# Optimization experiments

Measured on AMD Instinct MI355X. Metric: run time of the kernel, lower is better.

Reference implementation:

```python
import jax, jax.numpy as jnp
import numpy as np

N, E = 50000, 1600000
IN_DIM, HID, HEADS, DH, NCLS = 1280, 256, 4, 64, 6
NEG_SLOPE = 0.2
LN_EPS = 1e-5


def setup_inputs() -> dict:
    key = jax.random.key(0)
    ks = jax.random.split(key, 24)
    p = {}
    p['x'] = jax.random.normal(ks[0], (N, IN_DIM), dtype=jnp.float32)
    p['edge_index'] = jax.random.randint(ks[1], (2, E), 0, N, dtype=jnp.int64)
    s = 0.05
    p['W_in'] = jax.random.normal(ks[2], (IN_DIM, HID), dtype=jnp.float32) * s
    p['b_in'] = jnp.zeros((HID,), jnp.float32)
    for l in range(2):
        p[f'W_gat{l}'] = jax.random.normal(ks[3 + 6 * l], (HID, HEADS * DH), dtype=jnp.float32) * s
        p[f'att_src{l}'] = jax.random.normal(ks[4 + 6 * l], (HEADS, DH), dtype=jnp.float32) * s
        p[f'att_dst{l}'] = jax.random.normal(ks[5 + 6 * l], (HEADS, DH), dtype=jnp.float32) * s
        p[f'b_gat{l}'] = jnp.zeros((HEADS * DH,), jnp.float32)
        p[f'ln_g{l}'] = jnp.ones((HID,), jnp.float32)
        p[f'ln_b{l}'] = jnp.zeros((HID,), jnp.float32)
    p['W_c1'] = jax.random.normal(ks[20], (HID, HID // 2), dtype=jnp.float32) * s
    p['b_c1'] = jnp.zeros((HID // 2,), jnp.float32)
    p['W_c2'] = jax.random.normal(ks[21], (HID // 2, NCLS), dtype=jnp.float32) * s
    p['b_c2'] = jnp.zeros((NCLS,), jnp.float32)
    return p


def _layer_norm(h, g, b):
    mu = jnp.mean(h, axis=-1, keepdims=True)
    var = jnp.mean((h - mu) ** 2, axis=-1, keepdims=True)
    return (h - mu) * jax.lax.rsqrt(var + LN_EPS) * g + b


def _gat_conv(h, src, dst, W, a_src, a_dst, bias):
    # h: [N, HID] -> per-head projections [N, H, DH]
    xh = (h @ W).reshape(N, HEADS, DH)
    al_src = jnp.sum(xh * a_src, axis=-1)  # [N, H]
    al_dst = jnp.sum(xh * a_dst, axis=-1)  # [N, H]
    e = jax.nn.leaky_relu(al_src[src] + al_dst[dst], NEG_SLOPE)  # [E', H]
    # edge softmax over incoming edges of each destination node
    m = jax.ops.segment_max(e, dst, num_segments=N)
    e = jnp.exp(e - m[dst])
    denom = jax.ops.segment_sum(e, dst, num_segments=N)
    w = e / denom[dst]  # [E', H]
    msg = xh[src] * w[:, :, None]  # [E', H, DH]
    out = jax.ops.segment_sum(msg, dst, num_segments=N)  # [N, H, DH]
    return out.reshape(N, HEADS * DH) + bias


def reference(x, edge_index, W_in, b_in, W_gat0, att_src0, att_dst0, b_gat0, ln_g0, ln_b0,
              W_gat1, att_src1, att_dst1, b_gat1, ln_g1, ln_b1, W_c1, b_c1, W_c2, b_c2):
    # add self loops (PyG GATConv default)
    loop = jnp.arange(N, dtype=edge_index.dtype)
    src = jnp.concatenate([edge_index[0], loop])
    dst = jnp.concatenate([edge_index[1], loop])

    h = jax.nn.relu(x @ W_in + b_in)

    for (Wg, asrc, adst, bg, g, b) in ((W_gat0, att_src0, att_dst0, b_gat0, ln_g0, ln_b0),
                                       (W_gat1, att_src1, att_dst1, b_gat1, ln_g1, ln_b1)):
        h_new = _gat_conv(h, src, dst, Wg, asrc, adst, bg)
        h_new = jax.nn.relu(_layer_norm(h_new, g, b))
        h = h + h_new

    logits = jax.nn.relu(h @ W_c1 + b_c1) @ W_c2 + b_c2
    return logits
```

## Files before the change

### kernel.cpp

```cpp
#include <hip/hip_runtime.h>

#define NN 50000
#define EE 1600000
#define INDIM 1280
#define HID 256
#define HEADS 4
#define DHD 64
#define NCLS 6
#define NEG 0.2f
#define LNEPS 1e-5f

typedef __attribute__((ext_vector_type(8))) short short8;
typedef __attribute__((ext_vector_type(4))) float floatx4;

__device__ __forceinline__ unsigned short f2b(float f) {
    unsigned int u = __float_as_uint(f);
    u += 0x7FFF + ((u >> 16) & 1);
    return (unsigned short)(u >> 16);
}
__device__ __forceinline__ float b2f(unsigned short b) {
    return __uint_as_float(((unsigned int)b) << 16);
}

#define WAIT_LGKM0() __builtin_amdgcn_s_waitcnt(0xC07F)

__global__ void init_cnt_kernel(int* __restrict__ cnt) {
    int n = blockIdx.x * 256 + threadIdx.x;
    if (n < NN) cnt[n] = 1;
}

__global__ void count_edges_kernel(const int* __restrict__ dst, int* __restrict__ cnt) {
    int e = blockIdx.x * 256 + threadIdx.x;
    if (e < EE) atomicAdd(&cnt[dst[e]], 1);
}

__global__ __launch_bounds__(1024) void scan1_kernel(const int* __restrict__ cnt,
                                                     int* __restrict__ scanned,
                                                     int* __restrict__ chtot, int n) {
    __shared__ int wsum[16];
    int tid = threadIdx.x, lane = tid & 63, wv = tid >> 6;
    int i = blockIdx.x * 1024 + tid;
    int s = (i < n) ? cnt[i] : 0;
#pragma unroll
    for (int off = 1; off < 64; off <<= 1) {
        int t = __shfl_up(s, off, 64);
        if (lane >= off) s += t;
    }
    if (lane == 63) wsum[wv] = s;
    __syncthreads();
    if (tid < 16) {
        int ws = wsum[tid];
#pragma unroll
        for (int off = 1; off < 16; off <<= 1) {
            int t = __shfl_up(ws, off, 16);
            if (tid >= off) ws += t;
        }
        wsum[tid] = ws;
    }
    __syncthreads();
    s += (wv > 0) ? wsum[wv - 1] : 0;
    if (i < n) scanned[i] = s;
    if (tid == 1023) chtot[blockIdx.x] = s;
}

__global__ void scan2_kernel(int* __restrict__ chtot, int nch) {
    int lane = threadIdx.x;
    int v = (lane < nch) ? chtot[lane] : 0;
#pragma unroll
    for (int off = 1; off < 64; off <<= 1) {
        int t = __shfl_up(v, off, 64);
        if (lane >= off) v += t;
    }
    if (lane < nch) chtot[lane] = v;
}

__global__ void scan3_kernel(const int* __restrict__ scanned, const int* __restrict__ chtot,
                             int* __restrict__ rowptr, int n) {
    int i = blockIdx.x * 256 + threadIdx.x;
    if (i == 0) rowptr[0] = 0;
    if (i < n) {
        int ch = i >> 10;
        rowptr[i + 1] = scanned[i] + (ch ? chtot[ch - 1] : 0);
    }
}

__global__ void copyfill_kernel(const int* __restrict__ rowptr, int* __restrict__ cursor,
                                int* __restrict__ csr) {
    int n = blockIdx.x * 256 + threadIdx.x;
    if (n < NN) {
        int p = rowptr[n];
        csr[p] = n;
        cursor[n] = p + 1;
    }
}

__global__ void scatter_edges_kernel(const int* __restrict__ src, const int* __restrict__ dst,
                                     int* __restrict__ cursor, int* __restrict__ csr) {
    int e = blockIdx.x * 256 + threadIdx.x;
    if (e < EE) {
        int d = dst[e];
        int pos = atomicAdd(&cursor[d], 1);
        csr[pos] = src[e];
    }
}

__global__ void pack_w_kernel(const float* __restrict__ W, unsigned short* __restrict__ out,
                              int K, int N) {
    int idx = blockIdx.x * 256 + threadIdx.x;
    int total = (K >> 6) * (N >> 4) * 2 * 64;
    if (idx >= total) return;
    int ln = idx & 63;
    int t = idx >> 6;
    int ks = t & 1; t >>= 1;
    int NT = N >> 4;
    int nt = t % NT, kc = t / NT;
    int n = nt * 16 + (ln & 15);
    int k = kc * 64 + ks * 32 + ((ln >> 4) << 3);
    unsigned short u[8];
#pragma unroll
    for (int j = 0; j < 8; j++) u[j] = f2b(W[(size_t)(k + j) * N + n]);
    *(int4*)&out[(size_t)idx * 8] = *(const int4*)u;
}

template <int AF32, int KI, int NT, int ACT, int WF32, int WB16, int PROJ, int CLS>
__global__ __launch_bounds__(256) void pgemm_kernel(const float* __restrict__ Af,
                                                    const unsigned short* __restrict__ Ab,
                                                    const unsigned short* __restrict__ Bf,
                                                    const float* __restrict__ bias,
                                                    float* __restrict__ Cf,
                                                    unsigned short* __restrict__ Cb,
                                                    const float* __restrict__ aps,
                                                    const float* __restrict__ apd,
                                                    float* __restrict__ als,
                                                    float* __restrict__ ald,
                                                    const float* __restrict__ W2,
                                                    const float* __restrict__ b2,
                                                    float* __restrict__ out2,
                                                    int M) {
    constexpr int NW = NT / 4;
    constexpr int K = KI * 64;
    __shared__ __align__(16) unsigned short Als[2][4096];
    int tid = threadIdx.x, wv = tid >> 6, ln = tid & 63;
    int m0 = blockIdx.x * 64;

    int srow[2], scol[2];
#pragma unroll
    for (int i = 0; i < 2; i++) {
        int s = tid + i * 256;
        int r = s >> 3;
        srow[i] = min(m0 + r, M - 1);
        scol[i] = ((s & 7) ^ (r & 7)) * 8;
    }

    floatx4 acc[4][NW] = {};
    short8 breg[2][NW * 2];
    float4 af0[4], af1[4];
    int4 ai0[2], ai1[2];

    auto issueA = [&](int k, float4* af, int4* ai) {
#pragma unroll
        for (int i = 0; i < 2; i++) {
            if (AF32) {
                const float* p = Af + (size_t)srow[i] * K + k * 64 + scol[i];
                af[i * 2] = *(const float4*)p;
                af[i * 2 + 1] = *(const float4*)(p + 4);
            } else {
                ai[i] = *(const int4*)(Ab + (size_t)srow[i] * K + k * 64 + scol[i]);
            }
        }
    };
    auto issueB = [&](int k, short8* b) {
#pragma unroll
        for (int nw = 0; nw < NW; nw++)
#pragma unroll
            for (int ks = 0; ks < 2; ks++)
                b[nw * 2 + ks] = *(const short8*)(
                    Bf + ((((size_t)k * NT + (wv * NW + nw)) * 2 + ks) * 64 + ln) * 8);
    };
    auto writeA = [&](int k, const float4* af, const int4* ai) {
        unsigned short* dst = &Als[k & 1][0];
#pragma unroll
        for (int i = 0; i < 2; i++) {
            int4 v;
            if (AF32) {
                unsigned short u[8] = {f2b(af[2 * i].x), f2b(af[2 * i].y),
                                       f2b(af[2 * i].z), f2b(af[2 * i].w),
                                       f2b(af[2 * i + 1].x), f2b(af[2 * i + 1].y),
                                       f2b(af[2 * i + 1].z), f2b(af[2 * i + 1].w)};
                v = *(const int4*)u;
            } else {
                v = ai[i];
            }
            *(int4*)&dst[(tid + i * 256) * 8] = v;
        }
    };
    auto compute = [&](int k, const short8* b) {
        const unsigned short* src = &Als[k & 1][0];
#pragma unroll
        for (int ks = 0; ks < 2; ks++) {
            short8 a[4];
#pragma unroll
            for (int mt = 0; mt < 4; mt++) {
                int row = mt * 16 + (ln & 15);
                int g = ks * 4 + (ln >> 4);
                int off8 = (row >> 3) * 512 + (row & 7) * 64 + (g ^ (row & 7)) * 8;
                a[mt] = *(const short8*)&src[off8];
            }
#pragma unroll
            for (int nw = 0; nw < NW; nw++)
#pragma unroll
                for (int mt = 0; mt < 4; mt++)
                    acc[mt][nw] = __builtin_amdgcn_mfma_f32_16x16x32_bf16(
                        a[mt], b[nw * 2 + ks], acc[mt][nw], 0, 0, 0);
        }
    };

    issueA(0, af0, ai0);
    issueB(0, breg[0]);
    writeA(0, af0, ai0);
    WAIT_LGKM0();
    __builtin_amdgcn_s_barrier();

#pragma unroll
    for (int kk = 0; kk < KI / 2; kk++) {
        int k = kk * 2;
        issueA(k + 1, af1, ai1);
        issueB(k + 1, breg[1]);
        compute(k, breg[0]);
        writeA(k + 1, af1, ai1);
        WAIT_LGKM0();
        __builtin_amdgcn_s_barrier();
        if (k + 2 < KI) {
            issueA(k + 2, af0, ai0);
            issueB(k + 2, breg[0]);
        }
        compute(k + 1, breg[1]);
        if (k + 2 < KI) {
            writeA(k + 2, af0, ai0);
            WAIT_LGKM0();
            __builtin_amdgcn_s_barrier();
        }
    }

    constexpr int Nout = NT * 16;
    if constexpr (WF32 || WB16) {
#pragma unroll
        for (int mt = 0; mt < 4; mt++) {
#pragma unroll
            for (int nw = 0; nw < NW; nw++) {
                int col = (wv * NW + nw) * 16 + (ln & 15);
                int rb = m0 + mt * 16 + (ln >> 4) * 4;
                float bi = bias ? bias[col] : 0.f;
#pragma unroll
                for (int r = 0; r < 4; r++) {
                    int row = rb + r;
                    if (row < M) {
                        float v = acc[mt][nw][r] + bi;
                        if (ACT) v = fmaxf(v, 0.f);
                        if (WF32) Cf[(size_t)row * Nout + col] = v;
                        if (WB16) Cb[(size_t)row * Nout + col] = f2b(v);
                    }
                }
            }
        }
    }

    if constexpr (PROJ) {
        float avs[NW], avd[NW];
#pragma unroll
        for (int nw = 0; nw < NW; nw++) {
            int d = nw * 16 + (ln & 15);
            avs[nw] = aps[wv * DHD + d];
            avd[nw] = apd[wv * DHD + d];
        }
#pragma unroll
        for (int mt = 0; mt < 4; mt++) {
#pragma unroll
            for (int r = 0; r < 4; r++) {
                float ssum = 0.f, dsum = 0.f;
#pragma unroll
                for (int nw = 0; nw < NW; nw++) {
                    float v = acc[mt][nw][r];
                    ssum = fmaf(v, avs[nw], ssum);
                    dsum = fmaf(v, avd[nw], dsum);
                }
#pragma unroll
                for (int m = 8; m > 0; m >>= 1) {
                    ssum += __shfl_xor(ssum, m, 16);
                    dsum += __shfl_xor(dsum, m, 16);
                }
                int row = m0 + mt * 16 + (ln >> 4) * 4 + r;
                if ((ln & 15) == 0 && row < M) {
                    als[row * 4 + wv] = ssum;
                    ald[row * 4 + wv] = dsum;
                }
            }
        }
    }

    if constexpr (CLS) {
        __shared__ float cred[64][4][NCLS];
        float w2[NW][NCLS];
#pragma unroll
        for (int nw = 0; nw < NW; nw++) {
            int col = (wv * NW + nw) * 16 + (ln & 15);
#pragma unroll
            for (int c = 0; c < NCLS; c++) w2[nw][c] = W2[col * NCLS + c];
        }
#pragma unroll
        for (int mt = 0; mt < 4; mt++) {
#pragma unroll
            for (int r = 0; r < 4; r++) {
                float p[NCLS] = {};
#pragma unroll
                for (int nw = 0; nw < NW; nw++) {
                    int col = (wv * NW + nw) * 16 + (ln & 15);
                    float v = fmaxf(acc[mt][nw][r] + bias[col], 0.f);
#pragma unroll
                    for (int c = 0; c < NCLS; c++) p[c] = fmaf(v, w2[nw][c], p[c]);
                }
#pragma unroll
                for (int m = 8; m > 0; m >>= 1)
#pragma unroll
                    for (int c = 0; c < NCLS; c++) p[c] += __shfl_xor(p[c], m, 16);
                int rl = mt * 16 + (ln >> 4) * 4 + r;
                if ((ln & 15) == 0)
#pragma unroll
                    for (int c = 0; c < NCLS; c++) cred[rl][wv][c] = p[c];
            }
        }
        __syncthreads();
        for (int t = tid; t < 64 * NCLS; t += 256) {
            int row = t / NCLS, c = t % NCLS;
            if (m0 + row < M) {
                float s = cred[row][0][c] + cred[row][1][c] + cred[row][2][c] +
                          cred[row][3][c] + b2[c];
                out2[(size_t)(m0 + row) * NCLS + c] = s;
            }
        }
    }
}

__global__ __launch_bounds__(256) void agg_ln_kernel(const int* __restrict__ rowptr,
                                                     const int* __restrict__ csr,
                                                     const float* __restrict__ al_s,
                                                     const float* __restrict__ al_d,
                                                     const unsigned short* __restrict__ xhb,
                                                     const float* __restrict__ bgat,
                                                     const float* __restrict__ g,
                                                     const float* __restrict__ bb,
                                                     float* __restrict__ h,
                                                     unsigned short* __restrict__ hb) {
    int wv = threadIdx.x >> 6, ln = threadIdx.x & 63;
    int n = blockIdx.x * 4 + wv;
    if (n >= NN) return;
    int start = rowptr[n], end = rowptr[n + 1];
    float4 ad = *(const float4*)&al_d[n * 4];

    float d0 = 0.f, d1 = 0.f, d2 = 0.f, d3 = 0.f;
    for (int i = start + ln; i < end; i += 64) {
        int s = csr[i];
        float4 as = *(const float4*)&al_s[s * 4];
        float e0 = as.x + ad.x; e0 = e0 > 0.f ? e0 : NEG * e0;
        float e1 = as.y + ad.y; e1 = e1 > 0.f ? e1 : NEG * e1;
        float e2 = as.z + ad.z; e2 = e2 > 0.f ? e2 : NEG * e2;
        float e3 = as.w + ad.w; e3 = e3 > 0.f ? e3 : NEG * e3;
        d0 += __expf(e0); d1 += __expf(e1); d2 += __expf(e2); d3 += __expf(e3);
    }
#pragma unroll
    for (int off = 32; off > 0; off >>= 1) {
        d0 += __shfl_xor(d0, off, 64);
        d1 += __shfl_xor(d1, off, 64);
        d2 += __shfl_xor(d2, off, 64);
        d3 += __shfl_xor(d3, off, 64);
    }
    int myh = ln >> 4;
    float invh = 1.f / ((myh == 0) ? d0 : (myh == 1) ? d1 : (myh == 2) ? d2 : d3);
    float adh = (myh == 0) ? ad.x : (myh == 1) ? ad.y : (myh == 2) ? ad.z : ad.w;

    float p0 = 0.f, p1 = 0.f, p2 = 0.f, p3 = 0.f;
    float q0 = 0.f, q1 = 0.f, q2 = 0.f, q3 = 0.f;
    int i = start;
    for (; i + 1 < end; i += 2) {
        int s0 = csr[i], s1 = csr[i + 1];
        float e0 = al_s[s0 * 4 + myh] + adh; e0 = e0 > 0.f ? e0 : NEG * e0;
        float e1 = al_s[s1 * 4 + myh] + adh; e1 = e1 > 0.f ? e1 : NEG * e1;
        float w0 = __expf(e0) * invh;
        float w1 = __expf(e1) * invh;
        ushort4 u0 = *(const ushort4*)&xhb[(size_t)s0 * HID + ln * 4];
        ushort4 u1 = *(const ushort4*)&xhb[(size_t)s1 * HID + ln * 4];
        p0 = fmaf(w0, b2f(u0.x), p0); q0 = fmaf(w1, b2f(u1.x), q0);
        p1 = fmaf(w0, b2f(u0.y), p1); q1 = fmaf(w1, b2f(u1.y), q1);
        p2 = fmaf(w0, b2f(u0.z), p2); q2 = fmaf(w1, b2f(u1.z), q2);
        p3 = fmaf(w0, b2f(u0.w), p3); q3 = fmaf(w1, b2f(u1.w), q3);
    }
    if (i < end) {
        int s0 = csr[i];
        float e0 = al_s[s0 * 4 + myh] + adh; e0 = e0 > 0.f ? e0 : NEG * e0;
        float w0 = __expf(e0) * invh;
        ushort4 u0 = *(const ushort4*)&xhb[(size_t)s0 * HID + ln * 4];
        p0 = fmaf(w0, b2f(u0.x), p0);
        p1 = fmaf(w0, b2f(u0.y), p1);
        p2 = fmaf(w0, b2f(u0.z), p2);
        p3 = fmaf(w0, b2f(u0.w), p3);
    }
    float a0 = p0 + q0, a1 = p1 + q1, a2 = p2 + q2, a3 = p3 + q3;

    float4 bg = *(const float4*)&bgat[ln * 4];
    float v0 = a0 + bg.x, v1 = a1 + bg.y, v2 = a2 + bg.z, v3 = a3 + bg.w;
    float ps = v0 + v1 + v2 + v3;
    float ps2 = v0 * v0 + v1 * v1 + v2 * v2 + v3 * v3;
#pragma unroll
    for (int off = 32; off > 0; off >>= 1) {
        ps += __shfl_xor(ps, off, 64);
        ps2 += __shfl_xor(ps2, off, 64);
    }
    float mu = ps * (1.f / HID);
    float var = ps2 * (1.f / HID) - mu * mu;
    float rs = rsqrtf(var + LNEPS);
    float4 gg = *(const float4*)&g[ln * 4];
    float4 bbv = *(const float4*)&bb[ln * 4];
    float o0 = fmaxf((v0 - mu) * rs * gg.x + bbv.x, 0.f);
    float o1 = fmaxf((v1 - mu) * rs * gg.y + bbv.y, 0.f);
    float o2 = fmaxf((v2 - mu) * rs * gg.z + bbv.z, 0.f);
    float o3 = fmaxf((v3 - mu) * rs * gg.w + bbv.w, 0.f);
    size_t idx = (size_t)n * HID + ln * 4;
    float4 hv = *(const float4*)&h[idx];
    float4 nh = make_float4(hv.x + o0, hv.y + o1, hv.z + o2, hv.w + o3);
    *(float4*)&h[idx] = nh;
    ushort4 nb = {f2b(nh.x), f2b(nh.y), f2b(nh.z), f2b(nh.w)};
    *(ushort4*)&hb[idx] = nb;
}

extern "C" void kernel_launch(void* const* d_in, const int* in_sizes, int n_in,
                              void* d_out, int out_size, void* d_ws, size_t ws_size,
                              hipStream_t stream) {
    const float* x    = (const float*)d_in[0];
    const int*   ei   = (const int*)d_in[1];
    const float* W_in = (const float*)d_in[2];
    const float* b_in = (const float*)d_in[3];
    const float* W_gat[2]   = {(const float*)d_in[4],  (const float*)d_in[10]};
    const float* att_src[2] = {(const float*)d_in[5],  (const float*)d_in[11]};
    const float* att_dst[2] = {(const float*)d_in[6],  (const float*)d_in[12]};
    const float* b_gat[2]   = {(const float*)d_in[7],  (const float*)d_in[13]};
    const float* ln_g[2]    = {(const float*)d_in[8],  (const float*)d_in[14]};
    const float* ln_b[2]    = {(const float*)d_in[9],  (const float*)d_in[15]};
    const float* W_c1 = (const float*)d_in[16];
    const float* b_c1 = (const float*)d_in[17];
    const float* W_c2 = (const float*)d_in[18];
    const float* b_c2 = (const float*)d_in[19];

    char* ws = (char*)d_ws;
    size_t off = 0;
    auto alloc = [&](size_t bytes) -> void* {
        void* p = ws + off;
        off += (bytes + 255) & ~(size_t)255;
        return p;
    };
    float*          h   = (float*)alloc((size_t)NN * HID * 4);
    unsigned short* hb  = (unsigned short*)alloc((size_t)NN * HID * 2);
    unsigned short* xhb = (unsigned short*)alloc((size_t)NN * HID * 2);
    float* al_s = (float*)alloc((size_t)NN * HEADS * 4);
    float* al_d = (float*)alloc((size_t)NN * HEADS * 4);
    int* rowptr  = (int*)alloc((size_t)(NN + 1) * 4);
    int* cursor  = (int*)alloc((size_t)NN * 4);
    int* csr     = (int*)alloc((size_t)(EE + NN) * 4);
    int* scanned = (int*)alloc((size_t)NN * 4);
    int* chtot   = (int*)alloc(64 * 4);
    unsigned short* WinF = (unsigned short*)alloc((size_t)HID * INDIM * 2);
    unsigned short* WgF0 = (unsigned short*)alloc((size_t)HID * HID * 2);
    unsigned short* WgF1 = (unsigned short*)alloc((size_t)HID * HID * 2);
    unsigned short* Wc1F = (unsigned short*)alloc((size_t)(HID / 2) * HID * 2);
    unsigned short* WgF[2] = {WgF0, WgF1};

    const int* srcv = ei;
    const int* dstv = ei + EE;

    pack_w_kernel<<<(INDIM * HID / 8 + 255) / 256, 256, 0, stream>>>(W_in, WinF, INDIM, HID);
    pack_w_kernel<<<(HID * HID / 8 + 255) / 256, 256, 0, stream>>>(W_gat[0], WgF0, HID, HID);
    pack_w_kernel<<<(HID * HID / 8 + 255) / 256, 256, 0, stream>>>(W_gat[1], WgF1, HID, HID);
    pack_w_kernel<<<(HID * (HID / 2) / 8 + 255) / 256, 256, 0, stream>>>(W_c1, Wc1F, HID, HID / 2);

    int nch = (NN + 1023) / 1024;
    init_cnt_kernel<<<(NN + 255) / 256, 256, 0, stream>>>(cursor);
    count_edges_kernel<<<(EE + 255) / 256, 256, 0, stream>>>(dstv, cursor);
    scan1_kernel<<<nch, 1024, 0, stream>>>(cursor, scanned, chtot, NN);
    scan2_kernel<<<1, 64, 0, stream>>>(chtot, nch);
    scan3_kernel<<<(NN + 255) / 256, 256, 0, stream>>>(scanned, chtot, rowptr, NN);
    copyfill_kernel<<<(NN + 255) / 256, 256, 0, stream>>>(rowptr, cursor, csr);
    scatter_edges_kernel<<<(EE + 255) / 256, 256, 0, stream>>>(srcv, dstv, cursor, csr);

    int MB64 = (NN + 63) / 64;

    pgemm_kernel<1, 20, 16, 1, 1, 1, 0, 0><<<MB64, 256, 0, stream>>>(
        x, nullptr, WinF, b_in, h, hb,
        nullptr, nullptr, nullptr, nullptr, nullptr, nullptr, nullptr, NN);

    for (int l = 0; l < 2; l++) {
        pgemm_kernel<0, 4, 16, 0, 0, 1, 1, 0><<<MB64, 256, 0, stream>>>(
            nullptr, hb, WgF[l], nullptr, nullptr, xhb,
            att_src[l], att_dst[l], al_s, al_d, nullptr, nullptr, nullptr, NN);
        agg_ln_kernel<<<(NN + 3) / 4, 256, 0, stream>>>(rowptr, csr, al_s, al_d, xhb,
                                                        b_gat[l], ln_g[l], ln_b[l], h, hb);
    }

    pgemm_kernel<0, 4, 8, 1, 0, 0, 0, 1><<<MB64, 256, 0, stream>>>(
        nullptr, hb, Wc1F, b_c1, nullptr, nullptr,
        nullptr, nullptr, nullptr, nullptr, W_c2, b_c2, (float*)d_out, NN);
}
```

Baseline: 1.014 ms.

## Single-pass GAT aggregation with split-wave edges and deferred softmax normalization

The aggregation kernel no longer runs a separate pass over the edges to compute softmax denominators. It accumulates unnormalized weighted sums together with the denominator and divides once at the end. The wave is split into two halves that each take alternate edges, with 32 lanes covering the 256-wide row using 16-byte bf16 loads, and the halves are combined with cross-half shuffles. This removes the second read of csr and al_s and doubles the memory-level parallelism per wave. In exchange it adds shuffles and register pressure from 16 accumulators. The two halves split the output writes between them, one storing the fp32 h and the other the bf16 copy.

```diff
diff --git a/kernel.cpp b/kernel.cpp
--- a/kernel.cpp
+++ b/kernel.cpp
@@ -355,81 +355,95 @@
     int n = blockIdx.x * 4 + wv;
     if (n >= NN) return;
     int start = rowptr[n], end = rowptr[n + 1];
-    float4 ad = *(const float4*)&al_d[n * 4];
-
-    float d0 = 0.f, d1 = 0.f, d2 = 0.f, d3 = 0.f;
-    for (int i = start + ln; i < end; i += 64) {
-        int s = csr[i];
-        float4 as = *(const float4*)&al_s[s * 4];
-        float e0 = as.x + ad.x; e0 = e0 > 0.f ? e0 : NEG * e0;
-        float e1 = as.y + ad.y; e1 = e1 > 0.f ? e1 : NEG * e1;
-        float e2 = as.z + ad.z; e2 = e2 > 0.f ? e2 : NEG * e2;
-        float e3 = as.w + ad.w; e3 = e3 > 0.f ? e3 : NEG * e3;
-        d0 += __expf(e0); d1 += __expf(e1); d2 += __expf(e2); d3 += __expf(e3);
-    }
-#pragma unroll
-    for (int off = 32; off > 0; off >>= 1) {
-        d0 += __shfl_xor(d0, off, 64);
-        d1 += __shfl_xor(d1, off, 64);
-        d2 += __shfl_xor(d2, off, 64);
-        d3 += __shfl_xor(d3, off, 64);
-    }
-    int myh = ln >> 4;
-    float invh = 1.f / ((myh == 0) ? d0 : (myh == 1) ? d1 : (myh == 2) ? d2 : d3);
-    float adh = (myh == 0) ? ad.x : (myh == 1) ? ad.y : (myh == 2) ? ad.z : ad.w;
-
-    float p0 = 0.f, p1 = 0.f, p2 = 0.f, p3 = 0.f;
-    float q0 = 0.f, q1 = 0.f, q2 = 0.f, q3 = 0.f;
-    int i = start;
-    for (; i + 1 < end; i += 2) {
-        int s0 = csr[i], s1 = csr[i + 1];
-        float e0 = al_s[s0 * 4 + myh] + adh; e0 = e0 > 0.f ? e0 : NEG * e0;
-        float e1 = al_s[s1 * 4 + myh] + adh; e1 = e1 > 0.f ? e1 : NEG * e1;
-        float w0 = __expf(e0) * invh;
-        float w1 = __expf(e1) * invh;
-        ushort4 u0 = *(const ushort4*)&xhb[(size_t)s0 * HID + ln * 4];
-        ushort4 u1 = *(const ushort4*)&xhb[(size_t)s1 * HID + ln * 4];
-        p0 = fmaf(w0, b2f(u0.x), p0); q0 = fmaf(w1, b2f(u1.x), q0);
-        p1 = fmaf(w0, b2f(u0.y), p1); q1 = fmaf(w1, b2f(u1.y), q1);
-        p2 = fmaf(w0, b2f(u0.z), p2); q2 = fmaf(w1, b2f(u1.z), q2);
-        p3 = fmaf(w0, b2f(u0.w), p3); q3 = fmaf(w1, b2f(u1.w), q3);
+    int half = ln >> 5;
+    int j = ln & 31;
+    int head = j >> 3;
+    float adh = al_d[n * 4 + head];
+
+    float p[8] = {}, q[8] = {};
+    float dsp = 0.f, dsq = 0.f;
+
+    int i = start + half;
+    for (; i + 2 < end; i += 4) {
+        int s0 = csr[i], s1 = csr[i + 2];
+        float e0 = al_s[s0 * 4 + head] + adh; e0 = e0 > 0.f ? e0 : NEG * e0;
+        float e1 = al_s[s1 * 4 + head] + adh; e1 = e1 > 0.f ? e1 : NEG * e1;
+        float w0 = __expf(e0), w1 = __expf(e1);
+        dsp += w0; dsq += w1;
+        short8 u0 = *(const short8*)&xhb[(size_t)s0 * HID + j * 8];
+        short8 u1 = *(const short8*)&xhb[(size_t)s1 * HID + j * 8];
+#pragma unroll
+        for (int k = 0; k < 8; k++) {
+            p[k] = fmaf(w0, b2f((unsigned short)u0[k]), p[k]);
+            q[k] = fmaf(w1, b2f((unsigned short)u1[k]), q[k]);
+        }
     }
     if (i < end) {
         int s0 = csr[i];
-        float e0 = al_s[s0 * 4 + myh] + adh; e0 = e0 > 0.f ? e0 : NEG * e0;
-        float w0 = __expf(e0) * invh;
-        ushort4 u0 = *(const ushort4*)&xhb[(size_t)s0 * HID + ln * 4];
-        p0 = fmaf(w0, b2f(u0.x), p0);
-        p1 = fmaf(w0, b2f(u0.y), p1);
-        p2 = fmaf(w0, b2f(u0.z), p2);
-        p3 = fmaf(w0, b2f(u0.w), p3);
-    }
-    float a0 = p0 + q0, a1 = p1 + q1, a2 = p2 + q2, a3 = p3 + q3;
-
-    float4 bg = *(const float4*)&bgat[ln * 4];
-    float v0 = a0 + bg.x, v1 = a1 + bg.y, v2 = a2 + bg.z, v3 = a3 + bg.w;
-    float ps = v0 + v1 + v2 + v3;
-    float ps2 = v0 * v0 + v1 * v1 + v2 * v2 + v3 * v3;
-#pragma unroll
-    for (int off = 32; off > 0; off >>= 1) {
+        float e0 = al_s[s0 * 4 + head] + adh; e0 = e0 > 0.f ? e0 : NEG * e0;
+        float w0 = __expf(e0);
+        dsp += w0;
+        short8 u0 = *(const short8*)&xhb[(size_t)s0 * HID + j * 8];
+#pragma unroll
+        for (int k = 0; k < 8; k++) p[k] = fmaf(w0, b2f((unsigned short)u0[k]), p[k]);
+    }
+
+    float ds = dsp + dsq;
+    ds += __shfl_xor(ds, 32, 64);
+    float inv = 1.f / ds;
+
+    const float4* bgp = (const float4*)&bgat[j * 8];
+    float4 bg0 = bgp[0], bg1 = bgp[1];
+    float bgk[8] = {bg0.x, bg0.y, bg0.z, bg0.w, bg1.x, bg1.y, bg1.z, bg1.w};
+
+    float vv[8];
+    float ps = 0.f, ps2 = 0.f;
+#pragma unroll
+    for (int k = 0; k < 8; k++) {
+        float t = p[k] + q[k];
+        t += __shfl_xor(t, 32, 64);
+        float val = t * inv + bgk[k];
+        vv[k] = val;
+        ps += val;
+        ps2 = fmaf(val, val, ps2);
+    }
+#pragma unroll
+    for (int off = 16; off > 0; off >>= 1) {
         ps += __shfl_xor(ps, off, 64);
         ps2 += __shfl_xor(ps2, off, 64);
     }
     float mu = ps * (1.f / HID);
     float var = ps2 * (1.f / HID) - mu * mu;
     float rs = rsqrtf(var + LNEPS);
-    float4 gg = *(const float4*)&g[ln * 4];
-    float4 bbv = *(const float4*)&bb[ln * 4];
-    float o0 = fmaxf((v0 - mu) * rs * gg.x + bbv.x, 0.f);
-    float o1 = fmaxf((v1 - mu) * rs * gg.y + bbv.y, 0.f);
-    float o2 = fmaxf((v2 - mu) * rs * gg.z + bbv.z, 0.f);
-    float o3 = fmaxf((v3 - mu) * rs * gg.w + bbv.w, 0.f);
-    size_t idx = (size_t)n * HID + ln * 4;
-    float4 hv = *(const float4*)&h[idx];
-    float4 nh = make_float4(hv.x + o0, hv.y + o1, hv.z + o2, hv.w + o3);
-    *(float4*)&h[idx] = nh;
-    ushort4 nb = {f2b(nh.x), f2b(nh.y), f2b(nh.z), f2b(nh.w)};
-    *(ushort4*)&hb[idx] = nb;
+
+    const float4* gp = (const float4*)&g[j * 8];
+    const float4* bp = (const float4*)&bb[j * 8];
+    float4 g0 = gp[0], g1 = gp[1];
+    float4 c0 = bp[0], c1 = bp[1];
+    float gk[8] = {g0.x, g0.y, g0.z, g0.w, g1.x, g1.y, g1.z, g1.w};
+    float ck[8] = {c0.x, c0.y, c0.z, c0.w, c1.x, c1.y, c1.z, c1.w};
+
+    size_t idx = (size_t)n * HID + j * 8;
+    const float4* hp = (const float4*)&h[idx];
+    float4 h0 = hp[0], h1 = hp[1];
+    float hk[8] = {h0.x, h0.y, h0.z, h0.w, h1.x, h1.y, h1.z, h1.w};
+
+    float nh[8];
+#pragma unroll
+    for (int k = 0; k < 8; k++) {
+        float o = fmaxf((vv[k] - mu) * rs * gk[k] + ck[k], 0.f);
+        nh[k] = hk[k] + o;
+    }
+
+    if (half == 0) {
+        ((float4*)&h[idx])[0] = make_float4(nh[0], nh[1], nh[2], nh[3]);
+        ((float4*)&h[idx])[1] = make_float4(nh[4], nh[5], nh[6], nh[7]);
+    } else {
+        unsigned short ub[8];
+#pragma unroll
+        for (int k = 0; k < 8; k++) ub[k] = f2b(nh[k]);
+        *(int4*)&hb[idx] = *(const int4*)ub;
+    }
 }
 
 extern "C" void kernel_launch(void* const* d_in, const int* in_sizes, int n_in,
```

Measured after the change: 993.1 us. 1.02x faster.
